# Kernel tuning notes

Measured on AMD Instinct MI355X. Metric: run time of the kernel, lower is better.

The kernel has to match this reference:

```python
import jax, jax.numpy as jnp
import numpy as np

NUM_HEADS = 12
HEAD_DIM = 64
HIDDEN = NUM_HEADS * HEAD_DIM  # 768
B, L = 4, 512

def setup_inputs() -> dict:
    key = jax.random.key(0)
    ks = jax.random.split(key, 8)
    s = 0.02
    return {
        "hidden_states": jax.random.normal(ks[0], (B, L, HIDDEN), jnp.float32),
        "relation_embedding_k": jax.random.normal(ks[1], (B, L, L, HEAD_DIM), jnp.float32),
        "relation_embedding_v": jax.random.normal(ks[2], (B, L, L, HEAD_DIM), jnp.float32),
        "Wq": jax.random.normal(ks[3], (HIDDEN, HIDDEN), jnp.float32) * s,
        "bq": jnp.zeros((HIDDEN,), jnp.float32),
        "Wk": jax.random.normal(ks[4], (HIDDEN, HIDDEN), jnp.float32) * s,
        "bk": jnp.zeros((HIDDEN,), jnp.float32),
        "Wv": jax.random.normal(ks[5], (HIDDEN, HIDDEN), jnp.float32) * s,
        "bv": jnp.zeros((HIDDEN,), jnp.float32),
    }

def _heads(x):
    # [B, L, HIDDEN] -> [B, H, L, D]
    b, l, _ = x.shape
    return x.reshape(b, l, NUM_HEADS, HEAD_DIM).transpose(0, 2, 1, 3)

def reference(hidden_states, relation_embedding_k, relation_embedding_v,
              Wq, bq, Wk, bk, Wv, bv):
    q = _heads(hidden_states @ Wq + bq)  # [B,H,L,D]
    k = _heads(hidden_states @ Wk + bk)
    v = _heads(hidden_states @ Wv + bv)

    # content scores + relation key scores (shared across heads)
    scores = jnp.einsum('bhld,bhmd->bhlm', q, k)
    scores = scores + jnp.einsum('bhld,blrd->bhlr', q, relation_embedding_k)
    scores = scores / np.sqrt(HEAD_DIM).astype(np.float32)

    probs = jax.nn.softmax(scores, axis=-1)  # [B,H,L,L]

    ctx = jnp.einsum('bhlm,bhmd->bhld', probs, v)
    ctx = ctx + jnp.einsum('bhlr,brld->bhld', probs, relation_embedding_v)

    # [B,H,L,D] -> [B,L,HIDDEN]
    b, h, l, d = ctx.shape
    return ctx.transpose(0, 2, 1, 3).reshape(b, l, h * d)
```

## Files before the change

kernel.cpp:

```cpp
#include <hip/hip_runtime.h>
#include <stdint.h>


typedef __attribute__((ext_vector_type(8))) short bf16x8;
typedef __attribute__((ext_vector_type(4))) float f32x4;
typedef __attribute__((ext_vector_type(4))) unsigned int u32x4;
typedef __attribute__((ext_vector_type(2))) unsigned int u32x2;

__device__ __forceinline__ unsigned short f2bf(float f) {
  union { float f; unsigned int u; } v; v.f = f;
  unsigned int r = v.u + 0x7fffu + ((v.u >> 16) & 1u);
  return (unsigned short)(r >> 16);
}
__device__ __forceinline__ float bf2f(unsigned short s) {
  union { unsigned int u; float f; } v; v.u = ((unsigned int)s) << 16;
  return v.f;
}
__device__ __forceinline__ void lds_barrier() {
  asm volatile("s_waitcnt lgkmcnt(0)\ns_barrier" ::: "memory");
}
__device__ __forceinline__ unsigned cvtpk(float lo, float hi) {
  unsigned r;
  asm("v_cvt_pk_bf16_f32 %0, %1, %2" : "=v"(r) : "v"(lo), "v"(hi));
  return r;
}

#define GL16(dst, addr, OFF)                                                  \
  asm volatile("global_load_dwordx4 %0, %1, off offset:" #OFF                \
               : "=v"(dst) : "v"(addr))
#define WAITV(N)                                                              \
  do {                                                                        \
    asm volatile("s_waitcnt vmcnt(" #N ")" ::: "memory");                     \
    __builtin_amdgcn_sched_barrier(0);                                        \
  } while (0)

__global__ void k_cvt_hidden(const float* __restrict__ x, unsigned short* __restrict__ y) {
  int i = blockIdx.x * 256 + threadIdx.x;
  float4 v = reinterpret_cast<const float4*>(x)[i];
  ushort4 o;
  o.x = f2bf(v.x); o.y = f2bf(v.y); o.z = f2bf(v.z); o.w = f2bf(v.w);
  reinterpret_cast<ushort4*>(y)[i] = o;
}

__global__ void k_transp_w(const float* __restrict__ Wq, const float* __restrict__ Wk,
                           const float* __restrict__ Wv, unsigned short* __restrict__ wt) {
  __shared__ float t[64][65];
  const int kt = blockIdx.x, nt = blockIdx.y, wsel = blockIdx.z;
  const float* W = wsel == 0 ? Wq : (wsel == 1 ? Wk : Wv);
  const int lx = threadIdx.x & 63, ly = threadIdx.x >> 6;
  for (int i = 0; i < 64; i += 4)
    t[ly + i][lx] = W[(size_t)(kt * 64 + ly + i) * 768 + nt * 64 + lx];
  __syncthreads();
  for (int i = 0; i < 64; i += 4) {
    int r = ly + i;
    wt[((size_t)wsel * 768 + nt * 64 + r) * 768 + kt * 64 + lx] = f2bf(t[lx][r]);
  }
}

__global__ __launch_bounds__(256) void k_qkv_gemm(
    const unsigned short* __restrict__ A, const unsigned short* __restrict__ Bt,
    const float* __restrict__ bq, const float* __restrict__ bk, const float* __restrict__ bv,
    unsigned short* __restrict__ qbf, unsigned short* __restrict__ kbf,
    unsigned short* __restrict__ vbt) {
  __shared__ __align__(16) unsigned short lA[64 * 64];
  __shared__ __align__(16) unsigned short lB[64 * 64];
  const int tid = threadIdx.x, lane = tid & 63, w = tid >> 6;
  const int m0 = blockIdx.x * 64, n0 = blockIdx.y * 64;
  const int wm = (w >> 1) * 32, wn = (w & 1) * 32;
  f32x4 acc[2][2] = {};

  for (int kt = 0; kt < 12; ++kt) {
    __syncthreads();
#pragma unroll
    for (int i = 0; i < 2; ++i) {
      int e16 = i * 256 + tid;
      int row = e16 >> 3;
      int kb = (e16 & 7) * 16;
      int dst = row * 128 + (kb ^ ((row & 7) << 4));
      u32x4 va = *(const u32x4*)((const char*)A + (size_t)(m0 + row) * 1536 + kt * 128 + kb);
      *(u32x4*)((char*)lA + dst) = va;
      u32x4 vb = *(const u32x4*)((const char*)Bt + (size_t)(n0 + row) * 1536 + kt * 128 + kb);
      *(u32x4*)((char*)lB + dst) = vb;
    }
    __syncthreads();
#pragma unroll
    for (int ks = 0; ks < 2; ++ks) {
      bf16x8 fa[2], fb[2];
      const int kbyte = (ks * 32 + (lane >> 4) * 8) * 2;
#pragma unroll
      for (int mi = 0; mi < 2; ++mi) {
        int row = wm + mi * 16 + (lane & 15);
        fa[mi] = *(const bf16x8*)((const char*)lA + row * 128 + (kbyte ^ ((row & 7) << 4)));
      }
#pragma unroll
      for (int ni = 0; ni < 2; ++ni) {
        int row = wn + ni * 16 + (lane & 15);
        fb[ni] = *(const bf16x8*)((const char*)lB + row * 128 + (kbyte ^ ((row & 7) << 4)));
      }
#pragma unroll
      for (int mi = 0; mi < 2; ++mi)
#pragma unroll
        for (int ni = 0; ni < 2; ++ni)
          acc[mi][ni] = __builtin_amdgcn_mfma_f32_16x16x32_bf16(fa[mi], fb[ni], acc[mi][ni], 0, 0, 0);
    }
  }
#pragma unroll
  for (int mi = 0; mi < 2; ++mi)
#pragma unroll
    for (int ni = 0; ni < 2; ++ni) {
      int gn = n0 + wn + ni * 16 + (lane & 15);
      float bias = (gn < 768) ? bq[gn] : (gn < 1536 ? bk[gn - 768] : bv[gn - 1536]);
#pragma unroll
      for (int r = 0; r < 4; ++r) {
        int gm = m0 + wm + mi * 16 + ((lane >> 4) << 2) + r;
        float val = acc[mi][ni][r] + bias;
        int b = gm >> 9, l = gm & 511;
        int d = gn & 63;
        if (gn < 768) {
          int h = gn >> 6;
          qbf[(((size_t)(b * 12 + h)) * 512 + l) * 64 + d] = f2bf(val);
        } else if (gn < 1536) {
          int h = (gn - 768) >> 6;
          kbf[(((size_t)(b * 12 + h)) * 512 + l) * 64 + d] = f2bf(val);
        } else {
          int h = (gn - 1536) >> 6;
          vbt[(((size_t)(b * 12 + h)) * 64 + d) * 512 + l] = f2bf(val);
        }
      }
    }
}

__global__ __launch_bounds__(256) void k_scores(
    const unsigned short* __restrict__ qbf, const unsigned short* __restrict__ kbf,
    unsigned short* __restrict__ Sb) {
  __shared__ __align__(16) unsigned short lQ[64 * 64];
  __shared__ __align__(16) unsigned short lK[64 * 64];
  const int tid = threadIdx.x, lane = tid & 63, w = tid >> 6;
  const int mt = blockIdx.x, lt = blockIdx.y, bh = blockIdx.z;
  const int wm = (w >> 1) * 32, wn = (w & 1) * 32;
  f32x4 acc[2][2] = {};
#pragma unroll
  for (int i = 0; i < 2; ++i) {
    int e16 = i * 256 + tid;
    int row = e16 >> 3;
    int kb = (e16 & 7) * 16;
    int dst = row * 128 + (kb ^ ((row & 7) << 4));
    u32x4 vq = *(const u32x4*)((const char*)qbf + ((size_t)bh * 512 + lt * 64 + row) * 128 + kb);
    *(u32x4*)((char*)lQ + dst) = vq;
    u32x4 vk = *(const u32x4*)((const char*)kbf + ((size_t)bh * 512 + mt * 64 + row) * 128 + kb);
    *(u32x4*)((char*)lK + dst) = vk;
  }
  __syncthreads();
#pragma unroll
  for (int ks = 0; ks < 2; ++ks) {
    bf16x8 fa[2], fb[2];
    const int kbyte = (ks * 32 + (lane >> 4) * 8) * 2;
#pragma unroll
    for (int mi = 0; mi < 2; ++mi) {
      int row = wm + mi * 16 + (lane & 15);
      fa[mi] = *(const bf16x8*)((const char*)lQ + row * 128 + (kbyte ^ ((row & 7) << 4)));
    }
#pragma unroll
    for (int ni = 0; ni < 2; ++ni) {
      int row = wn + ni * 16 + (lane & 15);
      fb[ni] = *(const bf16x8*)((const char*)lK + row * 128 + (kbyte ^ ((row & 7) << 4)));
    }
#pragma unroll
    for (int mi = 0; mi < 2; ++mi)
#pragma unroll
      for (int ni = 0; ni < 2; ++ni)
        acc[mi][ni] = __builtin_amdgcn_mfma_f32_16x16x32_bf16(fa[mi], fb[ni], acc[mi][ni], 0, 0, 0);
  }
#pragma unroll
  for (int mi = 0; mi < 2; ++mi)
#pragma unroll
    for (int ni = 0; ni < 2; ++ni) {
      int gm = mt * 64 + wn + ni * 16 + (lane & 15);
#pragma unroll
      for (int r = 0; r < 4; ++r) {
        int gl = lt * 64 + wm + mi * 16 + ((lane >> 4) << 2) + r;
        Sb[(size_t)bh * 262144 + (size_t)gl * 512 + gm] = f2bf(acc[mi][ni][r]);
      }
    }
}

__global__ __launch_bounds__(256, 4) void k_relA(
    const unsigned short* __restrict__ qbf,
    const float* __restrict__ relk,
    const unsigned short* __restrict__ Sb,
    unsigned short* __restrict__ pbf) {
  __shared__ __align__(16) char X[24576];
  const int tid = threadIdx.x, lane = tid & 63, w = tid >> 6;
  const int bl = blockIdx.x, b = bl >> 9, l = bl & 511;
  const int lm = lane & 15, lg = lane >> 4;
  const int hq = lm < 12 ? lm : 11;

  union { f32x4 f; bf16x8 b; } qa0, qa1;
  const char* aQ = (const char*)qbf + (((size_t)b * 12 + hq) * 512 + l) * 128 + (size_t)lg * 16;
  GL16(qa0.f, aQ, 0);
  GL16(qa1.f, aQ, 64);

  const char* aA = (const char*)relk + (size_t)bl * 131072 +
                   (size_t)(w * 128 + lm) * 256 + (size_t)lg * 32;
  f32x4 td[3][4];
#define TISSUE(t, s)                                                          \
  do {                                                                        \
    const char* p_ = aA + (size_t)(t) * 4096;                                 \
    GL16(td[s][0], p_, 0);   GL16(td[s][1], p_, 16);                          \
    GL16(td[s][2], p_, 128); GL16(td[s][3], p_, 144);                         \
  } while (0)
#define ACONSUME(t, s)                                                        \
  do {                                                                        \
    union { bf16x8 v; unsigned u[4]; } fb0, fb1;                              \
    fb0.u[0] = cvtpk(td[s][0][0], td[s][0][1]);                               \
    fb0.u[1] = cvtpk(td[s][0][2], td[s][0][3]);                               \
    fb0.u[2] = cvtpk(td[s][1][0], td[s][1][1]);                               \
    fb0.u[3] = cvtpk(td[s][1][2], td[s][1][3]);                               \
    fb1.u[0] = cvtpk(td[s][2][0], td[s][2][1]);                               \
    fb1.u[1] = cvtpk(td[s][2][2], td[s][2][3]);                               \
    fb1.u[2] = cvtpk(td[s][3][0], td[s][3][1]);                               \
    fb1.u[3] = cvtpk(td[s][3][2], td[s][3][3]);                               \
    f32x4 acc = {0.f, 0.f, 0.f, 0.f};                                         \
    acc = __builtin_amdgcn_mfma_f32_16x16x32_bf16(qa0.b, fb0.v, acc, 0, 0, 0);\
    acc = __builtin_amdgcn_mfma_f32_16x16x32_bf16(qa1.b, fb1.v, acc, 0, 0, 0);\
    if (lg < 3) {                                                             \
      const int r_ = w * 128 + (t) * 16 + lm;                                 \
      _Pragma("unroll")                                                       \
      for (int reg = 0; reg < 4; ++reg)                                       \
        *(float*)(X + (lg * 4 + reg) * 2048 + ((r_ * 4) ^ (lg << 6))) =       \
            acc[reg];                                                         \
    }                                                                         \
  } while (0)

  TISSUE(0, 0); TISSUE(1, 1); TISSUE(2, 2);
  WAITV(8); ACONSUME(0, 0); TISSUE(3, 0);
  WAITV(8); ACONSUME(1, 1); TISSUE(4, 1);
  WAITV(8); ACONSUME(2, 2); TISSUE(5, 2);
  WAITV(8); ACONSUME(3, 0); TISSUE(6, 0);
  WAITV(8); ACONSUME(4, 1); TISSUE(7, 1);
  WAITV(8); ACONSUME(5, 2);
  WAITV(4); ACONSUME(6, 0);
  WAITV(0); ACONSUME(7, 1);
#undef TISSUE
#undef ACONSUME

  lds_barrier();

#pragma unroll
  for (int hh = 0; hh < 3; ++hh) {
    const int h = w * 3 + hh;
    const int sw = ((h >> 2) & 3) << 6;
    const size_t srow = (((size_t)b * 12 + h) * 512 + l) * 512;
    const unsigned short* sp = Sb + srow + lane;
    float sv[8];
    float mx = -1e30f;
#pragma unroll
    for (int j = 0; j < 8; ++j) {
      const int r = j * 64 + lane;
      float s = (*(const float*)(X + h * 2048 + ((r * 4) ^ sw)) + bf2f(sp[j * 64])) * 0.125f;
      sv[j] = s;
      mx = fmaxf(mx, s);
    }
#pragma unroll
    for (int off = 32; off; off >>= 1) mx = fmaxf(mx, __shfl_xor(mx, off));
    float sm = 0.f;
#pragma unroll
    for (int j = 0; j < 8; ++j) { sv[j] = __expf(sv[j] - mx); sm += sv[j]; }
#pragma unroll
    for (int off = 32; off; off >>= 1) sm += __shfl_xor(sm, off);
    const float inv = 1.f / sm;
#pragma unroll
    for (int j = 0; j < 8; ++j)
      pbf[srow + j * 64 + lane] = f2bf(sv[j] * inv);
  }
}

__global__ __launch_bounds__(256, 2) void k_relv(
    const unsigned short* __restrict__ pbf,
    const float* __restrict__ relv,
    unsigned short* __restrict__ part) {
  __shared__ __align__(16) char PS[49152];
  const int tid = threadIdx.x, lane = tid & 63, w = tid >> 6;
  const int lg = blockIdx.x, rc = blockIdx.y, b = blockIdx.z;
  const int l0 = lg * 16, r0 = rc * 128;

  {
    const int x = tid & 15, rowb = tid >> 4;
#pragma unroll
    for (int pass = 0; pass < 12; ++pass) {
      const int ri = pass * 16 + rowb;
      const int h = ri >> 4, lr = ri & 15;
      const char* src = (const char*)pbf +
          ((((size_t)b * 12 + h) * 512 + l0 + lr) * 512 + r0) * 2 + (size_t)x * 16;
      u32x4 v = *(const u32x4*)src;
      *(u32x4*)(PS + h * 4096 + lr * 256 + ((x * 16) ^ ((lr & 3) << 4))) = v;
    }
  }
  __syncthreads();

  const int lr_w = w * 4 + (lane >> 4);
  const int l = l0 + lr_w;
  const char* rvb = (const char*)relv +
      (((size_t)b * 512 + r0) * 512 + l) * 256 + (size_t)(lane & 15) * 16;

  f32x4 vA[8], vB[8], vC[8];
  f32x4 acc[12];
#pragma unroll
  for (int h = 0; h < 12; ++h) acc[h] = {0.f, 0.f, 0.f, 0.f};

#define VISSUE(o, buf)                                                        \
  do {                                                                        \
    GL16(buf[0], rvb + (size_t)((o) * 8 + 0) * 131072, 0);                    \
    GL16(buf[1], rvb + (size_t)((o) * 8 + 1) * 131072, 0);                    \
    GL16(buf[2], rvb + (size_t)((o) * 8 + 2) * 131072, 0);                    \
    GL16(buf[3], rvb + (size_t)((o) * 8 + 3) * 131072, 0);                    \
    GL16(buf[4], rvb + (size_t)((o) * 8 + 4) * 131072, 0);                    \
    GL16(buf[5], rvb + (size_t)((o) * 8 + 5) * 131072, 0);                    \
    GL16(buf[6], rvb + (size_t)((o) * 8 + 6) * 131072, 0);                    \
    GL16(buf[7], rvb + (size_t)((o) * 8 + 7) * 131072, 0);                    \
  } while (0)
#define VCONS(o, buf)                                                         \
  do {                                                                        \
    _Pragma("unroll")                                                         \
    for (int h = 0; h < 12; ++h) {                                            \
      bf16x8 p8 = *(const bf16x8*)(PS + h * 4096 + lr_w * 256 +               \
                                   (((o) * 16) ^ ((lr_w & 3) << 4)));         \
      _Pragma("unroll")                                                       \
      for (int j = 0; j < 8; ++j) {                                           \
        const float pf = bf2f((unsigned short)p8[j]);                         \
        acc[h] += pf * buf[j];                                                \
      }                                                                       \
    }                                                                         \
  } while (0)

  VISSUE(0, vA);
  VISSUE(1, vB);
  VISSUE(2, vC);
  WAITV(16); VCONS(0, vA);  VISSUE(3, vA);
  WAITV(16); VCONS(1, vB);  VISSUE(4, vB);
  WAITV(16); VCONS(2, vC);  VISSUE(5, vC);
  WAITV(16); VCONS(3, vA);  VISSUE(6, vA);
  WAITV(16); VCONS(4, vB);  VISSUE(7, vB);
  WAITV(16); VCONS(5, vC);  VISSUE(8, vC);
  WAITV(16); VCONS(6, vA);  VISSUE(9, vA);
  WAITV(16); VCONS(7, vB);  VISSUE(10, vB);
  WAITV(16); VCONS(8, vC);  VISSUE(11, vC);
  WAITV(16); VCONS(9, vA);  VISSUE(12, vA);
  WAITV(16); VCONS(10, vB); VISSUE(13, vB);
  WAITV(16); VCONS(11, vC); VISSUE(14, vC);
  WAITV(16); VCONS(12, vA); VISSUE(15, vA);
  WAITV(16); VCONS(13, vB);
  WAITV(8);  VCONS(14, vC);
  WAITV(0);  VCONS(15, vA);
#undef VISSUE
#undef VCONS

  unsigned short* op = part + ((size_t)rc * 2048 + (size_t)b * 512 + l) * 768 + (lane & 15) * 4;
#pragma unroll
  for (int h = 0; h < 12; ++h) {
    u32x2 pk;
    pk.x = cvtpk(acc[h][0], acc[h][1]);
    pk.y = cvtpk(acc[h][2], acc[h][3]);
    *(u32x2*)(op + h * 64) = pk;
  }
}

__global__ __launch_bounds__(256) void k_pv(
    const unsigned short* __restrict__ pbf, const unsigned short* __restrict__ vbt,
    const unsigned short* __restrict__ part, float* __restrict__ out) {
  __shared__ __align__(16) unsigned short lP[64 * 64];
  __shared__ __align__(16) unsigned short lV[64 * 64];
  const int tid = threadIdx.x, lane = tid & 63, w = tid >> 6;
  const int lt = blockIdx.x, bh = blockIdx.y;
  const int b = bh / 12, h = bh % 12;
  const int wm = (w >> 1) * 32, wn = (w & 1) * 32;
  f32x4 acc[2][2] = {};
  const char* pbase = (const char*)pbf + ((size_t)bh * 512 + lt * 64) * 1024;
  const char* vbase = (const char*)vbt + (size_t)bh * 64 * 1024;
  for (int kt = 0; kt < 8; ++kt) {
    __syncthreads();
#pragma unroll
    for (int i = 0; i < 2; ++i) {
      int e16 = i * 256 + tid;
      int row = e16 >> 3;
      int kb = (e16 & 7) * 16;
      int dst = row * 128 + (kb ^ ((row & 7) << 4));
      u32x4 vp = *(const u32x4*)(pbase + (size_t)row * 1024 + kt * 128 + kb);
      *(u32x4*)((char*)lP + dst) = vp;
      u32x4 vv = *(const u32x4*)(vbase + (size_t)row * 1024 + kt * 128 + kb);
      *(u32x4*)((char*)lV + dst) = vv;
    }
    __syncthreads();
#pragma unroll
    for (int ks = 0; ks < 2; ++ks) {
      bf16x8 fa[2], fb[2];
      const int kbyte = (ks * 32 + (lane >> 4) * 8) * 2;
#pragma unroll
      for (int mi = 0; mi < 2; ++mi) {
        int row = wm + mi * 16 + (lane & 15);
        fa[mi] = *(const bf16x8*)((const char*)lP + row * 128 + (kbyte ^ ((row & 7) << 4)));
      }
#pragma unroll
      for (int ni = 0; ni < 2; ++ni) {
        int row = wn + ni * 16 + (lane & 15);
        fb[ni] = *(const bf16x8*)((const char*)lV + row * 128 + (kbyte ^ ((row & 7) << 4)));
      }
#pragma unroll
      for (int mi = 0; mi < 2; ++mi)
#pragma unroll
        for (int ni = 0; ni < 2; ++ni)
          acc[mi][ni] = __builtin_amdgcn_mfma_f32_16x16x32_bf16(fa[mi], fb[ni], acc[mi][ni], 0, 0, 0);
    }
  }
#pragma unroll
  for (int mi = 0; mi < 2; ++mi)
#pragma unroll
    for (int ni = 0; ni < 2; ++ni) {
      int gd = wn + ni * 16 + (lane & 15);
#pragma unroll
      for (int r = 0; r < 4; ++r) {
        int gl = lt * 64 + wm + mi * 16 + ((lane >> 4) << 2) + r;
        size_t o = ((size_t)b * 512 + gl) * 768 + h * 64 + gd;
        out[o] = acc[mi][ni][r] + bf2f(part[o]) + bf2f(part[o + 1572864]) +
                 bf2f(part[o + 3145728]) + bf2f(part[o + 4718592]);
      }
    }
}

extern "C" void kernel_launch(void* const* d_in, const int* in_sizes, int n_in,
                              void* d_out, int out_size, void* d_ws, size_t ws_size,
                              hipStream_t stream) {
  (void)in_sizes; (void)n_in; (void)out_size; (void)ws_size;
  const float* hidden = (const float*)d_in[0];
  const float* relk   = (const float*)d_in[1];
  const float* relv   = (const float*)d_in[2];
  const float* Wq     = (const float*)d_in[3];
  const float* bq     = (const float*)d_in[4];
  const float* Wk     = (const float*)d_in[5];
  const float* bk     = (const float*)d_in[6];
  const float* Wv     = (const float*)d_in[7];
  const float* bv     = (const float*)d_in[8];
  float* out = (float*)d_out;
  char* ws = (char*)d_ws;

  unsigned short* hb  = (unsigned short*)(ws);
  unsigned short* wt  = (unsigned short*)(ws + 3145728);
  unsigned short* qbf = (unsigned short*)(ws + 6684672);
  unsigned short* kbf = (unsigned short*)(ws + 9830400);
  unsigned short* vbt = (unsigned short*)(ws + 12976128);
  unsigned short* Sb  = (unsigned short*)(ws + 16121856);
  unsigned short* part= (unsigned short*)(ws + 16121856);
  unsigned short* pbf = (unsigned short*)(ws + 66453504);

  k_cvt_hidden<<<1536, 256, 0, stream>>>(hidden, hb);
  k_transp_w<<<dim3(12, 12, 3), 256, 0, stream>>>(Wq, Wk, Wv, wt);
  k_qkv_gemm<<<dim3(32, 36), 256, 0, stream>>>(hb, wt, bq, bk, bv, qbf, kbf, vbt);
  k_scores<<<dim3(8, 8, 48), 256, 0, stream>>>(qbf, kbf, Sb);
  k_relA<<<2048, 256, 0, stream>>>(qbf, relk, Sb, pbf);
  k_relv<<<dim3(32, 4, 4), 256, 0, stream>>>(pbf, relv, part);
  k_pv<<<dim3(8, 48), 256, 0, stream>>>(pbf, vbt, part, out);
}
```

Measured before the change: 186.4 us.

## Split relv reduction into 8 chunks and prefetch score rows in relA

The relation-value kernel now handles 64 relation positions per block instead of 128. The grid grows to 8 r-chunks, LDS is halved and occupancy rises to 3 blocks per CU, using a two-buffer pipeline. The PV kernel sums 8 bf16 partials instead of 4, which adds extra partial traffic and workspace use. Separately, relA issues its content-score loads early as ushort global loads so they overlap the tail of the relation-key pipeline.

```diff
diff --git a/kernel.cpp b/kernel.cpp
--- a/kernel.cpp
+++ b/kernel.cpp
@@ -16,6 +16,10 @@
   union { unsigned int u; float f; } v; v.u = ((unsigned int)s) << 16;
   return v.f;
 }
+__device__ __forceinline__ float ubf(unsigned u) {
+  union { unsigned int u; float f; } v; v.u = u << 16;
+  return v.f;
+}
 __device__ __forceinline__ void lds_barrier() {
   asm volatile("s_waitcnt lgkmcnt(0)\ns_barrier" ::: "memory");
 }
@@ -27,6 +31,9 @@
 
 #define GL16(dst, addr, OFF)                                                  \
   asm volatile("global_load_dwordx4 %0, %1, off offset:" #OFF                \
+               : "=v"(dst) : "v"(addr))
+#define GLU(dst, addr, OFF)                                                   \
+  asm volatile("global_load_ushort %0, %1, off offset:" #OFF                 \
                : "=v"(dst) : "v"(addr))
 #define WAITV(N)                                                              \
   do {                                                                        \
@@ -232,32 +239,46 @@
     }                                                                         \
   } while (0)
 
+  unsigned sreg[3][8];
+  const char* aSb = (const char*)Sb +
+      (((((size_t)b * 12 + w * 3) * 512 + l) * 512) + lane) * 2;
+#define SRLOAD(hh)                                                            \
+  do {                                                                        \
+    const char* p_ = aSb + (size_t)(hh) * 524288;                             \
+    GLU(sreg[hh][0], p_, 0);   GLU(sreg[hh][1], p_, 128);                     \
+    GLU(sreg[hh][2], p_, 256); GLU(sreg[hh][3], p_, 384);                     \
+    GLU(sreg[hh][4], p_, 512); GLU(sreg[hh][5], p_, 640);                     \
+    GLU(sreg[hh][6], p_, 768); GLU(sreg[hh][7], p_, 896);                     \
+  } while (0)
+
   TISSUE(0, 0); TISSUE(1, 1); TISSUE(2, 2);
   WAITV(8); ACONSUME(0, 0); TISSUE(3, 0);
   WAITV(8); ACONSUME(1, 1); TISSUE(4, 1);
   WAITV(8); ACONSUME(2, 2); TISSUE(5, 2);
   WAITV(8); ACONSUME(3, 0); TISSUE(6, 0);
   WAITV(8); ACONSUME(4, 1); TISSUE(7, 1);
-  WAITV(8); ACONSUME(5, 2);
-  WAITV(4); ACONSUME(6, 0);
-  WAITV(0); ACONSUME(7, 1);
+  SRLOAD(0); SRLOAD(1); SRLOAD(2);
+  WAITV(32); ACONSUME(5, 2);
+  WAITV(28); ACONSUME(6, 0);
+  WAITV(24); ACONSUME(7, 1);
 #undef TISSUE
 #undef ACONSUME
+#undef SRLOAD
 
   lds_barrier();
+  WAITV(0);
 
 #pragma unroll
   for (int hh = 0; hh < 3; ++hh) {
     const int h = w * 3 + hh;
     const int sw = ((h >> 2) & 3) << 6;
     const size_t srow = (((size_t)b * 12 + h) * 512 + l) * 512;
-    const unsigned short* sp = Sb + srow + lane;
     float sv[8];
     float mx = -1e30f;
 #pragma unroll
     for (int j = 0; j < 8; ++j) {
       const int r = j * 64 + lane;
-      float s = (*(const float*)(X + h * 2048 + ((r * 4) ^ sw)) + bf2f(sp[j * 64])) * 0.125f;
+      float s = (*(const float*)(X + h * 2048 + ((r * 4) ^ sw)) + ubf(sreg[hh][j])) * 0.125f;
       sv[j] = s;
       mx = fmaxf(mx, s);
     }
@@ -275,25 +296,25 @@
   }
 }
 
-__global__ __launch_bounds__(256, 2) void k_relv(
+__global__ __launch_bounds__(256, 3) void k_relv(
     const unsigned short* __restrict__ pbf,
     const float* __restrict__ relv,
     unsigned short* __restrict__ part) {
-  __shared__ __align__(16) char PS[49152];
+  __shared__ __align__(16) char PS[24576];
   const int tid = threadIdx.x, lane = tid & 63, w = tid >> 6;
   const int lg = blockIdx.x, rc = blockIdx.y, b = blockIdx.z;
-  const int l0 = lg * 16, r0 = rc * 128;
+  const int l0 = lg * 16, r0 = rc * 64;
 
   {
-    const int x = tid & 15, rowb = tid >> 4;
-#pragma unroll
-    for (int pass = 0; pass < 12; ++pass) {
-      const int ri = pass * 16 + rowb;
+    const int x = tid & 7, rowb = tid >> 3;
+#pragma unroll
+    for (int pass = 0; pass < 6; ++pass) {
+      const int ri = pass * 32 + rowb;
       const int h = ri >> 4, lr = ri & 15;
       const char* src = (const char*)pbf +
           ((((size_t)b * 12 + h) * 512 + l0 + lr) * 512 + r0) * 2 + (size_t)x * 16;
       u32x4 v = *(const u32x4*)src;
-      *(u32x4*)(PS + h * 4096 + lr * 256 + ((x * 16) ^ ((lr & 3) << 4))) = v;
+      *(u32x4*)(PS + h * 2048 + lr * 128 + ((x * 16) ^ ((lr & 3) << 4))) = v;
     }
   }
   __syncthreads();
@@ -303,7 +324,7 @@
   const char* rvb = (const char*)relv +
       (((size_t)b * 512 + r0) * 512 + l) * 256 + (size_t)(lane & 15) * 16;
 
-  f32x4 vA[8], vB[8], vC[8];
+  f32x4 vA[8], vB[8];
   f32x4 acc[12];
 #pragma unroll
   for (int h = 0; h < 12; ++h) acc[h] = {0.f, 0.f, 0.f, 0.f};
@@ -323,7 +344,7 @@
   do {                                                                        \
     _Pragma("unroll")                                                         \
     for (int h = 0; h < 12; ++h) {                                            \
-      bf16x8 p8 = *(const bf16x8*)(PS + h * 4096 + lr_w * 256 +               \
+      bf16x8 p8 = *(const bf16x8*)(PS + h * 2048 + lr_w * 128 +               \
                                    (((o) * 16) ^ ((lr_w & 3) << 4)));         \
       _Pragma("unroll")                                                       \
       for (int j = 0; j < 8; ++j) {                                           \
@@ -335,23 +356,14 @@
 
   VISSUE(0, vA);
   VISSUE(1, vB);
-  VISSUE(2, vC);
-  WAITV(16); VCONS(0, vA);  VISSUE(3, vA);
-  WAITV(16); VCONS(1, vB);  VISSUE(4, vB);
-  WAITV(16); VCONS(2, vC);  VISSUE(5, vC);
-  WAITV(16); VCONS(3, vA);  VISSUE(6, vA);
-  WAITV(16); VCONS(4, vB);  VISSUE(7, vB);
-  WAITV(16); VCONS(5, vC);  VISSUE(8, vC);
-  WAITV(16); VCONS(6, vA);  VISSUE(9, vA);
-  WAITV(16); VCONS(7, vB);  VISSUE(10, vB);
-  WAITV(16); VCONS(8, vC);  VISSUE(11, vC);
-  WAITV(16); VCONS(9, vA);  VISSUE(12, vA);
-  WAITV(16); VCONS(10, vB); VISSUE(13, vB);
-  WAITV(16); VCONS(11, vC); VISSUE(14, vC);
-  WAITV(16); VCONS(12, vA); VISSUE(15, vA);
-  WAITV(16); VCONS(13, vB);
-  WAITV(8);  VCONS(14, vC);
-  WAITV(0);  VCONS(15, vA);
+  WAITV(8); VCONS(0, vA); VISSUE(2, vA);
+  WAITV(8); VCONS(1, vB); VISSUE(3, vB);
+  WAITV(8); VCONS(2, vA); VISSUE(4, vA);
+  WAITV(8); VCONS(3, vB); VISSUE(5, vB);
+  WAITV(8); VCONS(4, vA); VISSUE(6, vA);
+  WAITV(8); VCONS(5, vB); VISSUE(7, vB);
+  WAITV(8); VCONS(6, vA);
+  WAITV(0); VCONS(7, vB);
 #undef VISSUE
 #undef VCONS
 
@@ -421,8 +433,10 @@
       for (int r = 0; r < 4; ++r) {
         int gl = lt * 64 + wm + mi * 16 + ((lane >> 4) << 2) + r;
         size_t o = ((size_t)b * 512 + gl) * 768 + h * 64 + gd;
-        out[o] = acc[mi][ni][r] + bf2f(part[o]) + bf2f(part[o + 1572864]) +
-                 bf2f(part[o + 3145728]) + bf2f(part[o + 4718592]);
+        float s = acc[mi][ni][r];
+#pragma unroll
+        for (int k = 0; k < 8; ++k) s += bf2f(part[o + (size_t)k * 1572864]);
+        out[o] = s;
       }
     }
 }
@@ -457,6 +471,6 @@
   k_qkv_gemm<<<dim3(32, 36), 256, 0, stream>>>(hb, wt, bq, bk, bv, qbf, kbf, vbt);
   k_scores<<<dim3(8, 8, 48), 256, 0, stream>>>(qbf, kbf, Sb);
   k_relA<<<2048, 256, 0, stream>>>(qbf, relk, Sb, pbf);
-  k_relv<<<dim3(32, 4, 4), 256, 0, stream>>>(pbf, relv, part);
+  k_relv<<<dim3(32, 8, 4), 256, 0, stream>>>(pbf, relv, part);
   k_pv<<<dim3(8, 48), 256, 0, stream>>>(pbf, vbt, part, out);
 }
```

After: 190.7 us. 2.3% more time.

## Merge prep kernels and store relation scores as bf16 in LDS for occupancy

Applied to the files above, without the earlier changes.

Combines the hidden-state conversion and weight-transpose kernels into one launch, with block ID selecting the work, so one kernel launch goes away. In k_relA, the per-head relation-key scores are stored in LDS as bf16 rather than fp32, with the XOR swizzle adjusted to match. This halves the shared buffer and raises the launch-bounds occupancy hint from 4 to 5 blocks. The cost is extra rounding of the relation scores before softmax.

```diff
diff --git a/kernel.cpp b/kernel.cpp
--- a/kernel.cpp
+++ b/kernel.cpp
@@ -34,18 +34,23 @@
     __builtin_amdgcn_sched_barrier(0);                                        \
   } while (0)
 
-__global__ void k_cvt_hidden(const float* __restrict__ x, unsigned short* __restrict__ y) {
-  int i = blockIdx.x * 256 + threadIdx.x;
-  float4 v = reinterpret_cast<const float4*>(x)[i];
-  ushort4 o;
-  o.x = f2bf(v.x); o.y = f2bf(v.y); o.z = f2bf(v.z); o.w = f2bf(v.w);
-  reinterpret_cast<ushort4*>(y)[i] = o;
-}
-
-__global__ void k_transp_w(const float* __restrict__ Wq, const float* __restrict__ Wk,
-                           const float* __restrict__ Wv, unsigned short* __restrict__ wt) {
+__global__ void k_prep(const float* __restrict__ hidden,
+                       const float* __restrict__ Wq, const float* __restrict__ Wk,
+                       const float* __restrict__ Wv,
+                       unsigned short* __restrict__ hb,
+                       unsigned short* __restrict__ wt) {
   __shared__ float t[64][65];
-  const int kt = blockIdx.x, nt = blockIdx.y, wsel = blockIdx.z;
+  const int bid = blockIdx.x;
+  if (bid >= 432) {
+    int i = (bid - 432) * 256 + threadIdx.x;
+    float4 v = reinterpret_cast<const float4*>(hidden)[i];
+    ushort4 o;
+    o.x = f2bf(v.x); o.y = f2bf(v.y); o.z = f2bf(v.z); o.w = f2bf(v.w);
+    reinterpret_cast<ushort4*>(hb)[i] = o;
+    return;
+  }
+  const int wsel = bid / 144, rem = bid % 144;
+  const int kt = rem / 12, nt = rem % 12;
   const float* W = wsel == 0 ? Wq : (wsel == 1 ? Wk : Wv);
   const int lx = threadIdx.x & 63, ly = threadIdx.x >> 6;
   for (int i = 0; i < 64; i += 4)
@@ -184,12 +189,12 @@
     }
 }
 
-__global__ __launch_bounds__(256, 4) void k_relA(
+__global__ __launch_bounds__(256, 5) void k_relA(
     const unsigned short* __restrict__ qbf,
     const float* __restrict__ relk,
     const unsigned short* __restrict__ Sb,
     unsigned short* __restrict__ pbf) {
-  __shared__ __align__(16) char X[24576];
+  __shared__ __align__(16) char X[12288];
   const int tid = threadIdx.x, lane = tid & 63, w = tid >> 6;
   const int bl = blockIdx.x, b = bl >> 9, l = bl & 511;
   const int lm = lane & 15, lg = lane >> 4;
@@ -226,9 +231,12 @@
     if (lg < 3) {                                                             \
       const int r_ = w * 128 + (t) * 16 + lm;                                 \
       _Pragma("unroll")                                                       \
-      for (int reg = 0; reg < 4; ++reg)                                       \
-        *(float*)(X + (lg * 4 + reg) * 2048 + ((r_ * 4) ^ (lg << 6))) =       \
-            acc[reg];                                                         \
+      for (int reg = 0; reg < 4; ++reg) {                                     \
+        const int h_ = lg * 4 + reg;                                          \
+        *(unsigned short*)(X + h_ * 1024 +                                    \
+                           ((r_ * 2) ^ (((h_ >> 2) & 3) << 5))) =             \
+            f2bf(acc[reg]);                                                   \
+      }                                                                       \
     }                                                                         \
   } while (0)
 
@@ -249,7 +257,7 @@
 #pragma unroll
   for (int hh = 0; hh < 3; ++hh) {
     const int h = w * 3 + hh;
-    const int sw = ((h >> 2) & 3) << 6;
+    const int sw = ((h >> 2) & 3) << 5;
     const size_t srow = (((size_t)b * 12 + h) * 512 + l) * 512;
     const unsigned short* sp = Sb + srow + lane;
     float sv[8];
@@ -257,7 +265,8 @@
 #pragma unroll
     for (int j = 0; j < 8; ++j) {
       const int r = j * 64 + lane;
-      float s = (*(const float*)(X + h * 2048 + ((r * 4) ^ sw)) + bf2f(sp[j * 64])) * 0.125f;
+      float sr = bf2f(*(const unsigned short*)(X + h * 1024 + ((r * 2) ^ sw)));
+      float s = (sr + bf2f(sp[j * 64])) * 0.125f;
       sv[j] = s;
       mx = fmaxf(mx, s);
     }
@@ -452,8 +461,7 @@
   unsigned short* part= (unsigned short*)(ws + 16121856);
   unsigned short* pbf = (unsigned short*)(ws + 66453504);
 
-  k_cvt_hidden<<<1536, 256, 0, stream>>>(hidden, hb);
-  k_transp_w<<<dim3(12, 12, 3), 256, 0, stream>>>(Wq, Wk, Wv, wt);
+  k_prep<<<1968, 256, 0, stream>>>(hidden, Wq, Wk, Wv, hb, wt);
   k_qkv_gemm<<<dim3(32, 36), 256, 0, stream>>>(hb, wt, bq, bk, bv, qbf, kbf, vbt);
   k_scores<<<dim3(8, 8, 48), 256, 0, stream>>>(qbf, kbf, Sb);
   k_relA<<<2048, 256, 0, stream>>>(qbf, relk, Sb, pbf);
```

Result: faster. 181.2 us (median of 2 runs) (-2.8%).
